# Optimization experiments

Hardware: AMD Instinct MI355X
Metric: run time of the kernel (lower is better)

## Reference

```python
import jax, jax.numpy as jnp
import numpy as np

H = 512   # hidden_dim
K = 6     # n_subclusters
N = 4096  # number of stocks
C = 16    # current_n_clusters


def setup_inputs() -> dict:
    key = jax.random.key(0)
    ks = jax.random.split(key, 12)
    s = 1.0 / np.sqrt(H)
    inp = {
        "stock_embs": jax.random.normal(ks[0], (N, H), jnp.float32),
        "soft_cluster_weights": jax.random.uniform(ks[1], (N, C), jnp.float32),
        "latent_subsegment_assignments": jax.random.uniform(ks[2], (N, C, K), jnp.float32),
        "current_n_clusters": C,
        "Wq": jax.random.normal(ks[3], (H, H), jnp.float32) * s,
        "bq": jnp.zeros((H,), jnp.float32),
        "Wk": jax.random.normal(ks[4], (H, H), jnp.float32) * s,
        "bk": jnp.zeros((H,), jnp.float32),
        "Wv": jax.random.normal(ks[5], (H, H), jnp.float32) * s,
        "bv": jnp.zeros((H,), jnp.float32),
        "Wo": jax.random.normal(ks[6], (H, H), jnp.float32) * s,
        "bo": jnp.zeros((H,), jnp.float32),
        "ln_gamma": jnp.ones((K, H), jnp.float32),
        "ln_beta": jnp.zeros((K, H), jnp.float32),
    }
    return inp


def reference(stock_embs, soft_cluster_weights, latent_subsegment_assignments,
              current_n_clusters, Wq, bq, Wk, bk, Wv, bv, Wo, bo,
              ln_gamma, ln_beta):
    cc = current_n_clusters  # python int, static
    # Mask synthesis: sum_c (w_i w_j)(s_i s_j) == A_k @ A_k^T with A_k = w * s[:,:,k]
    A = soft_cluster_weights[:, :cc, None] * latent_subsegment_assignments[:, :cc, :]  # [N,cc,K]
    masks = jnp.einsum('nck,mck->knm', A, A)                      # [K,N,N]
    masks = masks / (jnp.max(masks, axis=(1, 2), keepdims=True) + 1e-8)
    masks = jnp.log(masks + 1e-10)

    # Projections (dropout is identity in eval mode)
    q = (stock_embs @ Wq.T + bq) / jnp.sqrt(jnp.float32(H))       # [N,H]
    k = stock_embs @ Wk.T + bk                                     # [N,H]
    v = stock_embs @ Wv.T + bv                                     # [N,H]
    scores = q @ k.T                                               # [N,N]

    attn = jax.nn.softmax(scores[None, :, :] + masks, axis=-1)     # [K,N,N]
    ctx = jnp.einsum('knm,md->knd', attn, v)                       # [K,N,H]
    out = ctx @ Wo.T + bo + stock_embs[None, :, :]                 # residual add

    # Per-subcluster LayerNorm (eps=1e-12)
    mu = jnp.mean(out, axis=-1, keepdims=True)
    var = jnp.mean((out - mu) ** 2, axis=-1, keepdims=True)
    out = (out - mu) / jnp.sqrt(var + 1e-12)
    out = out * ln_gamma[:, None, :] + ln_beta[:, None, :]         # [K,N,H]
    return out
```

## Files before the change

### kernel.cpp

```cpp
#include <hip/hip_runtime.h>


typedef _Float16 f16;
typedef _Float16 v8h __attribute__((ext_vector_type(8)));
typedef _Float16 v4h __attribute__((ext_vector_type(4)));
typedef float f32x4 __attribute__((ext_vector_type(4)));

#define MFMA_F16(a, b, c) __builtin_amdgcn_mfma_f32_16x16x32_f16(a, b, c, 0, 0, 0)

#define GLOAD16(gp, lp)                                                        \
  __builtin_amdgcn_global_load_lds(                                            \
      (const __attribute__((address_space(1))) void*)(gp),                     \
      (__attribute__((address_space(3))) void*)(lp), 16, 0, 0)


__global__ void cvt_f16_kernel(const float* __restrict__ in, f16* __restrict__ out, int n4) {
  int i = blockIdx.x * blockDim.x + threadIdx.x;
  if (i < n4) {
    float4 v = ((const float4*)in)[i];
    v4h o = {(f16)v.x, (f16)v.y, (f16)v.z, (f16)v.w};
    ((v4h*)out)[i] = o;
  }
}

__global__ void build_A_kernel(const float* __restrict__ wgt, const float* __restrict__ lat,
                               const int* __restrict__ ccp, f16* __restrict__ Ab, int total) {
  int idx = blockIdx.x * blockDim.x + threadIdx.x;
  if (idx >= total) return;
  int cc = ccp[0];
  int k = idx >> 17;
  int rem = idx & 131071;
  int n = rem >> 5;
  int c = rem & 31;
  float v = 0.f;
  if (c < cc) v = wgt[n * 16 + c] * lat[(n * 16 + c) * 6 + k];
  Ab[idx] = (f16)v;
}

__global__ void diag_max_kernel(const f16* __restrict__ Ab, unsigned* __restrict__ gmax) {
  int idx = blockIdx.x * 256 + threadIdx.x;
  int kk = idx >> 12;
  const v8h* p = (const v8h*)(Ab + (size_t)idx * 32);
  float s = 0.f;
#pragma unroll
  for (int q = 0; q < 4; ++q) {
    v8h a = p[q];
#pragma unroll
    for (int j = 0; j < 8; ++j) s += (float)a[j] * (float)a[j];
  }
#pragma unroll
  for (int msk = 1; msk < 64; msk <<= 1) s = fmaxf(s, __shfl_xor(s, msk, 64));
  if ((threadIdx.x & 63) == 0) atomicMax(&gmax[kk], __float_as_uint(s));
}


template <int MODE>
__global__ __launch_bounds__(256, 2) void gemm_bt(
    const f16* __restrict__ A, const f16* __restrict__ B,
    const float* __restrict__ bias, const float* __restrict__ resid,
    float* __restrict__ outf, f16* __restrict__ outh,
    int M, int Nn, int Kd, int ldo, float alpha) {
  __shared__ f16 As[128 * 32];
  __shared__ f16 Bs[128 * 32];
  const int t = threadIdx.x;
  const int w = t >> 6, lane = t & 63, r15 = lane & 15, r4 = lane >> 4;
  const int wr = w >> 1, wc = w & 1;
  const int row0 = blockIdx.x * 128, col0 = blockIdx.y * 128;

  f32x4 acc[4][4] = {};
  const f16* Ap = A + (size_t)(row0 + (t >> 2)) * Kd + (t & 3) * 8;
  const f16* Bp = B + (size_t)(col0 + (t >> 2)) * Kd + (t & 3) * 8;

  for (int k0 = 0; k0 < Kd; k0 += 32) {
    __syncthreads();
    GLOAD16(Ap + k0, &As[t * 8]);
    GLOAD16(Ap + k0 + (size_t)64 * Kd, &As[2048 + t * 8]);
    GLOAD16(Bp + k0, &Bs[t * 8]);
    GLOAD16(Bp + k0 + (size_t)64 * Kd, &Bs[2048 + t * 8]);
    __syncthreads();
    v8h a[4], b[4];
#pragma unroll
    for (int f = 0; f < 4; ++f) a[f] = *(const v8h*)&As[(wr * 64 + f * 16 + r15) * 32 + r4 * 8];
#pragma unroll
    for (int f = 0; f < 4; ++f) b[f] = *(const v8h*)&Bs[(wc * 64 + f * 16 + r15) * 32 + r4 * 8];
#pragma unroll
    for (int i = 0; i < 4; ++i)
#pragma unroll
      for (int j = 0; j < 4; ++j) acc[i][j] = MFMA_F16(a[i], b[j], acc[i][j]);
  }

#pragma unroll
  for (int i = 0; i < 4; ++i) {
#pragma unroll
    for (int j = 0; j < 4; ++j) {
#pragma unroll
      for (int r = 0; r < 4; ++r) {
        int row = row0 + wr * 64 + i * 16 + r4 * 4 + r;
        int col = col0 + wc * 64 + j * 16 + r15;
        float v = acc[i][j][r];
        if constexpr (MODE == 0) {
          outh[(size_t)row * ldo + col] = (f16)((v + bias[col]) * alpha);
        } else if constexpr (MODE == 1) {
          float vv = v + bias[col];
          size_t idx = (size_t)col * 4096 + (size_t)(row & ~31) + (size_t)((row & 31) ^ ((col & 3) << 3));
          outh[idx] = (f16)vv;
        } else if constexpr (MODE == 3) {
          outf[(size_t)row * ldo + col] = v + bias[col] + resid[(size_t)(row & 4095) * ldo + col];
        } else {
          outh[(size_t)row * ldo + col] = (f16)v;
        }
      }
    }
  }
}

__global__ __launch_bounds__(256) void rowmax_exp_kernel(const f16* __restrict__ scores,
                                                         f16* __restrict__ Eexp) {
  const int row = blockIdx.x, t = threadIdx.x;
  const v8h* src = (const v8h*)(scores + (size_t)row * 4096);
  v8h v0 = src[t], v1 = src[t + 256];
  float m = -3.4e38f;
#pragma unroll
  for (int j = 0; j < 8; ++j) m = fmaxf(m, fmaxf((float)v0[j], (float)v1[j]));
#pragma unroll
  for (int msk = 1; msk < 64; msk <<= 1) m = fmaxf(m, __shfl_xor(m, msk, 64));
  __shared__ float red[4];
  const int w = t >> 6, lane = t & 63;
  if (lane == 0) red[w] = m;
  __syncthreads();
  m = fmaxf(fmaxf(red[0], red[1]), fmaxf(red[2], red[3]));
  v8h o0, o1;
#pragma unroll
  for (int j = 0; j < 8; ++j) {
    o0[j] = (f16)__expf((float)v0[j] - m);
    o1[j] = (f16)__expf((float)v1[j] - m);
  }
  v8h* dst = (v8h*)(Eexp + (size_t)row * 4096);
  dst[t] = o0;
  dst[t + 256] = o1;
}

__global__ __launch_bounds__(512, 2) void attn_pv_kernel(
    const f16* __restrict__ Eexp, const f16* __restrict__ VT,
    const f16* __restrict__ Ab, const unsigned* __restrict__ gmax,
    f16* __restrict__ ctx) {
  __shared__ f16 Vt_s[512 * 32];
  __shared__ f16 E_s[64 * 32];
  __shared__ f16 P_s[64 * 32];
  __shared__ f16 Ar_s[64 * 32];
  __shared__ f16 Ac_s[32 * 32];
  __shared__ float denom_s[128];

  const int t = threadIdx.x;
  const int w = t >> 6, lane = t & 63, r15 = lane & 15, r4 = lane >> 4;
  const int fn = w & 3, fm = w >> 2;

  int d = blockIdx.x + gridDim.x * blockIdx.y;
  int l = (d & 7) * 48 + (d >> 3);
  int r_tile = l / 6;
  int kk = l - r_tile * 6;
  const int row0 = r_tile * 64;

  const float inv = 1.f / (__uint_as_float(gmax[kk]) + 1e-8f);

  f32x4 acc[4][4] = {};
  float dpart[4] = {0.f, 0.f, 0.f, 0.f};
  f32x4 zero4 = {};

  if (t < 256)
    GLOAD16(Ab + ((size_t)(kk * 4096 + row0 + (t >> 2))) * 32 + (t & 3) * 8, &Ar_s[t * 8]);

  for (int mc = 0; mc < 128; ++mc) {
    const int m0 = mc * 32;
#pragma unroll
    for (int i = 0; i < 4; ++i)
      GLOAD16(VT + ((size_t)(i * 128 + (t >> 2))) * 4096 + m0 + (t & 3) * 8, &Vt_s[i * 4096 + t * 8]);
    if (t < 256)
      GLOAD16(Eexp + ((size_t)(row0 + (t >> 2))) * 4096 + m0 + (t & 3) * 8, &E_s[t * 8]);
    if (t < 128)
      GLOAD16(Ab + ((size_t)(kk * 4096 + m0 + (t >> 2))) * 32 + (t & 3) * 8, &Ac_s[t * 8]);
    __syncthreads();
    v8h ga = *(const v8h*)&Ar_s[(fn * 16 + r15) * 32 + r4 * 8];
    v8h gb = *(const v8h*)&Ac_s[(fm * 16 + r15) * 32 + r4 * 8];
    f32x4 g = MFMA_F16(ga, gb, zero4);
#pragma unroll
    for (int r = 0; r < 4; ++r) {
      int nl = fn * 16 + r4 * 4 + r;
      int ml = fm * 16 + r15;
      float e = (float)E_s[nl * 32 + ml];
      float p = e * (g[r] * inv + 1e-10f);
      dpart[r] += p;
      P_s[nl * 32 + (ml ^ ((nl & 3) << 3))] = (f16)p;
    }
    __syncthreads();
    v8h pa[4], vb[4];
#pragma unroll
    for (int f = 0; f < 4; ++f) {
      int n2 = f * 16 + r15;
      pa[f] = *(const v8h*)&P_s[n2 * 32 + ((r4 * 8) ^ ((n2 & 3) << 3))];
      int hl = w * 64 + f * 16 + r15;
      vb[f] = *(const v8h*)&Vt_s[hl * 32 + ((r4 * 8) ^ ((hl & 3) << 3))];
    }
#pragma unroll
    for (int i = 0; i < 4; ++i)
#pragma unroll
      for (int j = 0; j < 4; ++j) acc[i][j] = MFMA_F16(pa[i], vb[j], acc[i][j]);
    __syncthreads();
  }

#pragma unroll
  for (int r = 0; r < 4; ++r) {
#pragma unroll
    for (int msk = 1; msk < 16; msk <<= 1) dpart[r] += __shfl_xor(dpart[r], msk, 64);
  }
  if (r15 == 0) {
#pragma unroll
    for (int r = 0; r < 4; ++r) denom_s[fm * 64 + fn * 16 + r4 * 4 + r] = dpart[r];
  }
  __syncthreads();
#pragma unroll
  for (int i = 0; i < 4; ++i) {
#pragma unroll
    for (int r = 0; r < 4; ++r) {
      int n = i * 16 + r4 * 4 + r;
      float invd = 1.f / (denom_s[n] + denom_s[64 + n]);
#pragma unroll
      for (int j = 0; j < 4; ++j) {
        ctx[((size_t)(kk * 4096 + row0 + n)) * 512 + w * 64 + j * 16 + r15] =
            (f16)(acc[i][j][r] * invd);
      }
    }
  }
}

__global__ __launch_bounds__(256) void ln_kernel(float* __restrict__ out,
                                                 const float* __restrict__ g,
                                                 const float* __restrict__ b) {
  const int row = blockIdx.x, t = threadIdx.x;
  const int k = row >> 12;
  float* base = out + (size_t)row * 512;
  float2 x = ((float2*)base)[t];
  float s = x.x + x.y, sq = x.x * x.x + x.y * x.y;
#pragma unroll
  for (int m = 1; m < 64; m <<= 1) {
    s += __shfl_xor(s, m, 64);
    sq += __shfl_xor(sq, m, 64);
  }
  __shared__ float S[4], Q[4];
  const int w = t >> 6, lane = t & 63;
  if (lane == 0) { S[w] = s; Q[w] = sq; }
  __syncthreads();
  s = S[0] + S[1] + S[2] + S[3];
  sq = Q[0] + Q[1] + Q[2] + Q[3];
  float mu = s * (1.f / 512.f);
  float var = sq * (1.f / 512.f) - mu * mu;
  float invs = rsqrtf(var + 1e-12f);
  int c0 = 2 * t, c1 = 2 * t + 1;
  float2 y;
  y.x = (x.x - mu) * invs * g[k * 512 + c0] + b[k * 512 + c0];
  y.y = (x.y - mu) * invs * g[k * 512 + c1] + b[k * 512 + c1];
  ((float2*)base)[t] = y;
}

extern "C" void kernel_launch(void* const* d_in, const int* in_sizes, int n_in,
                              void* d_out, int out_size, void* d_ws, size_t ws_size,
                              hipStream_t stream) {
  const float* embs = (const float*)d_in[0];
  const float* scw = (const float*)d_in[1];
  const float* lat = (const float*)d_in[2];
  const int* ccp = (const int*)d_in[3];
  const float* Wq = (const float*)d_in[4];
  const float* bq = (const float*)d_in[5];
  const float* Wk = (const float*)d_in[6];
  const float* bk = (const float*)d_in[7];
  const float* Wv = (const float*)d_in[8];
  const float* bv = (const float*)d_in[9];
  const float* Wo = (const float*)d_in[10];
  const float* bo = (const float*)d_in[11];
  const float* lng = (const float*)d_in[12];
  const float* lnb = (const float*)d_in[13];
  float* out = (float*)d_out;

  char* wsp = (char*)d_ws;
  f16* Eh = (f16*)(wsp);
  f16* Wqh = (f16*)(wsp + 0x400000);
  f16* Wkh = (f16*)(wsp + 0x480000);
  f16* Wvh = (f16*)(wsp + 0x500000);
  f16* Woh = (f16*)(wsp + 0x580000);
  f16* qh = (f16*)(wsp + 0x600000);
  f16* kh = (f16*)(wsp + 0xA00000);
  f16* VT = (f16*)(wsp + 0xE00000);
  f16* Ab = (f16*)(wsp + 0x1200000);
  unsigned* gmax = (unsigned*)(wsp + 0x1380000);
  f16* scores_h = (f16*)(wsp + 0x1400000);
  f16* ctxh = (f16*)(wsp + 0x1400000);
  f16* Eexp = (f16*)(wsp + 0x3400000);

  dim3 b256(256);

  cvt_f16_kernel<<<2048, b256, 0, stream>>>(embs, Eh, 524288);
  cvt_f16_kernel<<<256, b256, 0, stream>>>(Wq, Wqh, 65536);
  cvt_f16_kernel<<<256, b256, 0, stream>>>(Wk, Wkh, 65536);
  cvt_f16_kernel<<<256, b256, 0, stream>>>(Wv, Wvh, 65536);
  cvt_f16_kernel<<<256, b256, 0, stream>>>(Wo, Woh, 65536);
  build_A_kernel<<<3072, b256, 0, stream>>>(scw, lat, ccp, Ab, 786432);
  hipMemsetAsync(gmax, 0, 64, stream);

  const float qscale = 0.044194173824159216f;
  gemm_bt<0><<<dim3(32, 4), b256, 0, stream>>>(Eh, Wqh, bq, nullptr, nullptr, qh,
                                               4096, 512, 512, 512, qscale);
  gemm_bt<0><<<dim3(32, 4), b256, 0, stream>>>(Eh, Wkh, bk, nullptr, nullptr, kh,
                                               4096, 512, 512, 512, 1.f);
  gemm_bt<1><<<dim3(32, 4), b256, 0, stream>>>(Eh, Wvh, bv, nullptr, nullptr, VT,
                                               4096, 512, 512, 512, 1.f);
  gemm_bt<4><<<dim3(32, 32), b256, 0, stream>>>(qh, kh, nullptr, nullptr, nullptr, scores_h,
                                                4096, 4096, 512, 4096, 1.f);
  diag_max_kernel<<<96, b256, 0, stream>>>(Ab, gmax);
  rowmax_exp_kernel<<<4096, b256, 0, stream>>>(scores_h, Eexp);
  attn_pv_kernel<<<dim3(64, 6), 512, 0, stream>>>(Eexp, VT, Ab, gmax, ctxh);
  gemm_bt<3><<<dim3(192, 4), b256, 0, stream>>>(ctxh, Woh, bo, embs, out, nullptr,
                                                24576, 512, 512, 512, 1.f);
  ln_kernel<<<24576, b256, 0, stream>>>(out, lng, lnb);
}
```

Before: 420.6 us.

## Fuse conversions, QKV projections, diag-max, and Wo+LayerNorm; double-buffer attention kernel

```diff
diff --git a/kernel.cpp b/kernel.cpp
--- a/kernel.cpp
+++ b/kernel.cpp
@@ -13,20 +13,56 @@
       (const __attribute__((address_space(1))) void*)(gp),                     \
       (__attribute__((address_space(3))) void*)(lp), 16, 0, 0)
 
-
-__global__ void cvt_f16_kernel(const float* __restrict__ in, f16* __restrict__ out, int n4) {
-  int i = blockIdx.x * blockDim.x + threadIdx.x;
-  if (i < n4) {
-    float4 v = ((const float4*)in)[i];
+#define FENCE asm volatile("" ::: "memory")
+#define WAIT_LGKM0                                                             \
+  {                                                                            \
+    asm volatile("s_waitcnt lgkmcnt(0)" ::: "memory");                         \
+    __builtin_amdgcn_sched_barrier(0);                                         \
+  }
+#define WAIT_VM0                                                               \
+  {                                                                            \
+    asm volatile("s_waitcnt vmcnt(0)" ::: "memory");                           \
+    __builtin_amdgcn_sched_barrier(0);                                         \
+  }
+#define BARRIER                                                                \
+  {                                                                            \
+    FENCE;                                                                     \
+    __builtin_amdgcn_s_barrier();                                              \
+    FENCE;                                                                     \
+    __builtin_amdgcn_sched_barrier(0);                                         \
+  }
+
+__global__ void cvt_all_kernel(const float* __restrict__ embs,
+                               const float* __restrict__ Wq, const float* __restrict__ Wk,
+                               const float* __restrict__ Wv, const float* __restrict__ Wo,
+                               const float* __restrict__ bq, const float* __restrict__ bk,
+                               const float* __restrict__ bv,
+                               f16* __restrict__ Eh, f16* __restrict__ Wcat,
+                               float* __restrict__ bcat) {
+  int i = blockIdx.x * 256 + threadIdx.x;
+  if (i < 524288) {
+    float4 v = ((const float4*)embs)[i];
     v4h o = {(f16)v.x, (f16)v.y, (f16)v.z, (f16)v.w};
-    ((v4h*)out)[i] = o;
+    ((v4h*)Eh)[i] = o;
+  } else if (i < 786432) {
+    int widx = i - 524288;
+    int r = widx >> 16;
+    const float* src = (r == 0) ? Wq : (r == 1) ? Wk : (r == 2) ? Wv : Wo;
+    float4 v = ((const float4*)src)[widx & 65535];
+    v4h o = {(f16)v.x, (f16)v.y, (f16)v.z, (f16)v.w};
+    ((v4h*)Wcat)[widx] = o;
+  } else if (i < 786816) {
+    int bidx = i - 786432;
+    int r = bidx >> 7;
+    const float* src = (r == 0) ? bq : (r == 1) ? bk : bv;
+    ((float4*)bcat)[bidx] = ((const float4*)src)[bidx & 127];
   }
 }
 
 __global__ void build_A_kernel(const float* __restrict__ wgt, const float* __restrict__ lat,
-                               const int* __restrict__ ccp, f16* __restrict__ Ab, int total) {
-  int idx = blockIdx.x * blockDim.x + threadIdx.x;
-  if (idx >= total) return;
+                               const int* __restrict__ ccp, f16* __restrict__ Ab,
+                               unsigned* __restrict__ gmax) {
+  int idx = blockIdx.x * 256 + threadIdx.x;
   int cc = ccp[0];
   int k = idx >> 17;
   int rem = idx & 131071;
@@ -34,32 +70,28 @@
   int c = rem & 31;
   float v = 0.f;
   if (c < cc) v = wgt[n * 16 + c] * lat[(n * 16 + c) * 6 + k];
-  Ab[idx] = (f16)v;
-}
-
-__global__ void diag_max_kernel(const f16* __restrict__ Ab, unsigned* __restrict__ gmax) {
-  int idx = blockIdx.x * 256 + threadIdx.x;
-  int kk = idx >> 12;
-  const v8h* p = (const v8h*)(Ab + (size_t)idx * 32);
-  float s = 0.f;
-#pragma unroll
-  for (int q = 0; q < 4; ++q) {
-    v8h a = p[q];
-#pragma unroll
-    for (int j = 0; j < 8; ++j) s += (float)a[j] * (float)a[j];
-  }
-#pragma unroll
-  for (int msk = 1; msk < 64; msk <<= 1) s = fmaxf(s, __shfl_xor(s, msk, 64));
-  if ((threadIdx.x & 63) == 0) atomicMax(&gmax[kk], __float_as_uint(s));
-}
-
+  f16 h = (f16)v;
+  Ab[idx] = h;
+  float fv = (float)h;
+  float s = fv * fv;
+#pragma unroll
+  for (int m = 1; m <= 16; m <<= 1) s += __shfl_xor(s, m, 64);
+  s = fmaxf(s, __shfl_xor(s, 32, 64));
+  __shared__ float red[4];
+  int t = threadIdx.x, w = t >> 6;
+  if ((t & 63) == 0) red[w] = s;
+  __syncthreads();
+  if (t == 0) {
+    float m4 = fmaxf(fmaxf(red[0], red[1]), fmaxf(red[2], red[3]));
+    atomicMax(&gmax[k], __float_as_uint(m4));
+  }
+}
 
 template <int MODE>
 __global__ __launch_bounds__(256, 2) void gemm_bt(
     const f16* __restrict__ A, const f16* __restrict__ B,
-    const float* __restrict__ bias, const float* __restrict__ resid,
-    float* __restrict__ outf, f16* __restrict__ outh,
-    int M, int Nn, int Kd, int ldo, float alpha) {
+    const float* __restrict__ bias, f16* __restrict__ outh, f16* __restrict__ aux,
+    int Kd, int ldo, float alpha) {
   __shared__ f16 As[128 * 32];
   __shared__ f16 Bs[128 * 32];
   const int t = threadIdx.x;
@@ -98,16 +130,19 @@
         int row = row0 + wr * 64 + i * 16 + r4 * 4 + r;
         int col = col0 + wc * 64 + j * 16 + r15;
         float v = acc[i][j][r];
-        if constexpr (MODE == 0) {
-          outh[(size_t)row * ldo + col] = (f16)((v + bias[col]) * alpha);
-        } else if constexpr (MODE == 1) {
+        if constexpr (MODE == 4) {
+          outh[(size_t)row * ldo + col] = (f16)v;
+        } else {
           float vv = v + bias[col];
-          size_t idx = (size_t)col * 4096 + (size_t)(row & ~31) + (size_t)((row & 31) ^ ((col & 3) << 3));
-          outh[idx] = (f16)vv;
-        } else if constexpr (MODE == 3) {
-          outf[(size_t)row * ldo + col] = v + bias[col] + resid[(size_t)(row & 4095) * ldo + col];
-        } else {
-          outh[(size_t)row * ldo + col] = (f16)v;
+          int reg = col >> 9;
+          if (reg < 2) {
+            float sc = (reg == 0) ? alpha : 1.f;
+            outh[(size_t)reg * 2097152 + (size_t)row * 512 + (col & 511)] = (f16)(vv * sc);
+          } else {
+            int cv = col & 511;
+            aux[(size_t)cv * 4096 + (size_t)(row & ~31) + (size_t)((row & 31) ^ ((cv & 3) << 3))] =
+                (f16)vv;
+          }
         }
       }
     }
@@ -140,72 +175,99 @@
   dst[t + 256] = o1;
 }
 
-__global__ __launch_bounds__(512, 2) void attn_pv_kernel(
+__global__ __launch_bounds__(256, 3) void attn_pv2_kernel(
     const f16* __restrict__ Eexp, const f16* __restrict__ VT,
     const f16* __restrict__ Ab, const unsigned* __restrict__ gmax,
     f16* __restrict__ ctx) {
-  __shared__ f16 Vt_s[512 * 32];
-  __shared__ f16 E_s[64 * 32];
+  __shared__ f16 Vt_s[2][256 * 32];
+  __shared__ f16 E_s[2][64 * 32];
   __shared__ f16 P_s[64 * 32];
-  __shared__ f16 Ar_s[64 * 32];
-  __shared__ f16 Ac_s[32 * 32];
-  __shared__ float denom_s[128];
+  __shared__ float denom_s[64];
 
   const int t = threadIdx.x;
   const int w = t >> 6, lane = t & 63, r15 = lane & 15, r4 = lane >> 4;
-  const int fn = w & 3, fm = w >> 2;
-
-  int d = blockIdx.x + gridDim.x * blockIdx.y;
-  int l = (d & 7) * 48 + (d >> 3);
-  int r_tile = l / 6;
-  int kk = l - r_tile * 6;
-  const int row0 = r_tile * 64;
+
+  int d = blockIdx.x;
+  int xcd = d & 7, jj6 = d >> 3;
+  int strip = xcd * 8 + jj6 / 12;
+  int sub = jj6 % 12;
+  int hh = sub / 6, kk = sub - (sub / 6) * 6;
+  const int row0 = strip * 64;
+  const int h0 = hh * 256;
 
   const float inv = 1.f / (__uint_as_float(gmax[kk]) + 1e-8f);
+  const f16* Abk = Ab + (size_t)kk * 4096 * 32;
+
+  v8h ga = *(const v8h*)(Abk + (size_t)(row0 + w * 16 + r15) * 32 + r4 * 8);
 
   f32x4 acc[4][4] = {};
   float dpart[4] = {0.f, 0.f, 0.f, 0.f};
   f32x4 zero4 = {};
 
-  if (t < 256)
-    GLOAD16(Ab + ((size_t)(kk * 4096 + row0 + (t >> 2))) * 32 + (t & 3) * 8, &Ar_s[t * 8]);
-
-  for (int mc = 0; mc < 128; ++mc) {
-    const int m0 = mc * 32;
-#pragma unroll
-    for (int i = 0; i < 4; ++i)
-      GLOAD16(VT + ((size_t)(i * 128 + (t >> 2))) * 4096 + m0 + (t & 3) * 8, &Vt_s[i * 4096 + t * 8]);
-    if (t < 256)
-      GLOAD16(Eexp + ((size_t)(row0 + (t >> 2))) * 4096 + m0 + (t & 3) * 8, &E_s[t * 8]);
-    if (t < 128)
-      GLOAD16(Ab + ((size_t)(kk * 4096 + m0 + (t >> 2))) * 32 + (t & 3) * 8, &Ac_s[t * 8]);
-    __syncthreads();
-    v8h ga = *(const v8h*)&Ar_s[(fn * 16 + r15) * 32 + r4 * 8];
-    v8h gb = *(const v8h*)&Ac_s[(fm * 16 + r15) * 32 + r4 * 8];
-    f32x4 g = MFMA_F16(ga, gb, zero4);
-#pragma unroll
-    for (int r = 0; r < 4; ++r) {
-      int nl = fn * 16 + r4 * 4 + r;
-      int ml = fm * 16 + r15;
-      float e = (float)E_s[nl * 32 + ml];
-      float p = e * (g[r] * inv + 1e-10f);
-      dpart[r] += p;
-      P_s[nl * 32 + (ml ^ ((nl & 3) << 3))] = (f16)p;
-    }
-    __syncthreads();
-    v8h pa[4], vb[4];
-#pragma unroll
-    for (int f = 0; f < 4; ++f) {
-      int n2 = f * 16 + r15;
-      pa[f] = *(const v8h*)&P_s[n2 * 32 + ((r4 * 8) ^ ((n2 & 3) << 3))];
-      int hl = w * 64 + f * 16 + r15;
-      vb[f] = *(const v8h*)&Vt_s[hl * 32 + ((r4 * 8) ^ ((hl & 3) << 3))];
-    }
-#pragma unroll
-    for (int i = 0; i < 4; ++i)
-#pragma unroll
-      for (int j = 0; j < 4; ++j) acc[i][j] = MFMA_F16(pa[i], vb[j], acc[i][j]);
-    __syncthreads();
+#define ATTN_STAGE(P, M0S)                                                     \
+  {                                                                            \
+    _Pragma("unroll") for (int i2 = 0; i2 < 4; ++i2)                           \
+        GLOAD16(VT + (size_t)(h0 + i2 * 64 + (t >> 2)) * 4096 + (M0S) + (t & 3) * 8, \
+                &Vt_s[P][i2 * 2048 + t * 8]);                                  \
+    {                                                                          \
+      int nn = t >> 2;                                                         \
+      int cs = (t & 3) ^ ((nn >> 2) & 3);                                      \
+      GLOAD16(Eexp + (size_t)(row0 + nn) * 4096 + (M0S) + cs * 8, &E_s[P][t * 8]); \
+    }                                                                          \
+  }
+
+#define ATTN_COMPUTE(P, GB)                                                    \
+  {                                                                            \
+    f32x4 g0 = MFMA_F16(ga, GB[0], zero4);                                     \
+    f32x4 g1 = MFMA_F16(ga, GB[1], zero4);                                     \
+    _Pragma("unroll") for (int r = 0; r < 4; ++r) {                            \
+      int nl = w * 16 + r4 * 4 + r;                                            \
+      int xo = r4 << 3;                                                        \
+      float e0 = (float)E_s[P][nl * 32 + (r15 ^ xo)];                          \
+      float e1 = (float)E_s[P][nl * 32 + ((16 + r15) ^ xo)];                   \
+      float p0 = e0 * (g0[r] * inv + 1e-10f);                                  \
+      float p1 = e1 * (g1[r] * inv + 1e-10f);                                  \
+      dpart[r] += p0 + p1;                                                     \
+      P_s[nl * 32 + (r15 ^ xo)] = (f16)p0;                                     \
+      P_s[nl * 32 + ((16 + r15) ^ xo)] = (f16)p1;                              \
+    }                                                                          \
+    WAIT_LGKM0;                                                                \
+    BARRIER;                                                                   \
+    v8h pa[4], vb[4];                                                          \
+    _Pragma("unroll") for (int f = 0; f < 4; ++f) {                            \
+      int n2 = f * 16 + r15;                                                   \
+      pa[f] = *(const v8h*)&P_s[n2 * 32 + ((r4 * 8) ^ (((n2 >> 2) & 3) << 3))];\
+      int hl = w * 64 + f * 16 + r15;                                          \
+      vb[f] = *(const v8h*)&Vt_s[P][hl * 32 + ((r4 * 8) ^ ((hl & 3) << 3))];   \
+    }                                                                          \
+    __builtin_amdgcn_s_setprio(1);                                             \
+    _Pragma("unroll") for (int i = 0; i < 4; ++i)                              \
+        _Pragma("unroll") for (int j2 = 0; j2 < 4; ++j2)                       \
+            acc[i][j2] = MFMA_F16(pa[i], vb[j2], acc[i][j2]);                  \
+    __builtin_amdgcn_s_setprio(0);                                             \
+    WAIT_LGKM0;                                                                \
+    WAIT_VM0;                                                                  \
+    BARRIER;                                                                   \
+  }
+
+  ATTN_STAGE(0, 0);
+  v8h gb0[2], gb1[2];
+  gb0[0] = *(const v8h*)(Abk + (size_t)(0 + r15) * 32 + r4 * 8);
+  gb0[1] = *(const v8h*)(Abk + (size_t)(16 + r15) * 32 + r4 * 8);
+  WAIT_VM0;
+  BARRIER;
+
+  for (int mc = 0; mc < 128; mc += 2) {
+    int mn = (mc + 1) * 32;
+    ATTN_STAGE(1, mn);
+    gb1[0] = *(const v8h*)(Abk + (size_t)(mn + r15) * 32 + r4 * 8);
+    gb1[1] = *(const v8h*)(Abk + (size_t)(mn + 16 + r15) * 32 + r4 * 8);
+    ATTN_COMPUTE(0, gb0);
+    int mn2 = (mc + 2 < 128) ? (mc + 2) * 32 : 0;
+    ATTN_STAGE(0, mn2);
+    gb0[0] = *(const v8h*)(Abk + (size_t)(mn2 + r15) * 32 + r4 * 8);
+    gb0[1] = *(const v8h*)(Abk + (size_t)(mn2 + 16 + r15) * 32 + r4 * 8);
+    ATTN_COMPUTE(1, gb1);
   }
 
 #pragma unroll
@@ -215,7 +277,7 @@
   }
   if (r15 == 0) {
 #pragma unroll
-    for (int r = 0; r < 4; ++r) denom_s[fm * 64 + fn * 16 + r4 * 4 + r] = dpart[r];
+    for (int r = 0; r < 4; ++r) denom_s[w * 16 + r4 * 4 + r] = dpart[r];
   }
   __syncthreads();
 #pragma unroll
@@ -223,43 +285,144 @@
 #pragma unroll
     for (int r = 0; r < 4; ++r) {
       int n = i * 16 + r4 * 4 + r;
-      float invd = 1.f / (denom_s[n] + denom_s[64 + n]);
+      float invd = 1.f / denom_s[n];
 #pragma unroll
       for (int j = 0; j < 4; ++j) {
-        ctx[((size_t)(kk * 4096 + row0 + n)) * 512 + w * 64 + j * 16 + r15] =
+        ctx[((size_t)(kk * 4096 + row0 + n)) * 512 + h0 + w * 64 + j * 16 + r15] =
             (f16)(acc[i][j][r] * invd);
       }
     }
   }
-}
-
-__global__ __launch_bounds__(256) void ln_kernel(float* __restrict__ out,
-                                                 const float* __restrict__ g,
-                                                 const float* __restrict__ b) {
-  const int row = blockIdx.x, t = threadIdx.x;
-  const int k = row >> 12;
-  float* base = out + (size_t)row * 512;
-  float2 x = ((float2*)base)[t];
-  float s = x.x + x.y, sq = x.x * x.x + x.y * x.y;
-#pragma unroll
-  for (int m = 1; m < 64; m <<= 1) {
-    s += __shfl_xor(s, m, 64);
-    sq += __shfl_xor(sq, m, 64);
-  }
-  __shared__ float S[4], Q[4];
-  const int w = t >> 6, lane = t & 63;
-  if (lane == 0) { S[w] = s; Q[w] = sq; }
+#undef ATTN_STAGE
+#undef ATTN_COMPUTE
+}
+
+__global__ __launch_bounds__(512, 4) void wo_ln_kernel(
+    const f16* __restrict__ ctxh, const f16* __restrict__ Woh,
+    const float* __restrict__ bo, const float* __restrict__ embs,
+    const float* __restrict__ lng, const float* __restrict__ lnb,
+    float* __restrict__ out) {
+  __shared__ f16 As_[2][48 * 32];
+  __shared__ f16 Bs_[2][512 * 32];
+  __shared__ float redS[8][48];
+  __shared__ float redQ[8][48];
+  __shared__ float muS[48], ivS[48];
+
+  const int t = threadIdx.x;
+  const int w = t >> 6, lane = t & 63, r15 = lane & 15, r4 = lane >> 4;
+  const int row0 = blockIdx.x * 48;
+  const int wm3 = w % 3;
+  const int caRow = wm3 * 64 + lane;
+
+  f32x4 acc[3][4] = {};
+
+#define WO_STAGE(P, KQ)                                                        \
+  {                                                                            \
+    GLOAD16(ctxh + (size_t)(row0 + (caRow >> 2)) * 512 + (KQ) + (caRow & 3) * 8, \
+            &As_[P][caRow * 8]);                                               \
+    _Pragma("unroll") for (int q2 = 0; q2 < 4; ++q2)                           \
+        GLOAD16(Woh + (size_t)((q2 * 512 + t) >> 2) * 512 + (KQ) + (t & 3) * 8,\
+                &Bs_[P][(q2 * 512 + t) * 8]);                                  \
+  }
+
+#define WO_COMPUTE(P)                                                          \
+  {                                                                            \
+    v8h a[3], b[4];                                                            \
+    _Pragma("unroll") for (int i = 0; i < 3; ++i)                              \
+        a[i] = *(const v8h*)&As_[P][(i * 16 + r15) * 32 + r4 * 8];             \
+    _Pragma("unroll") for (int j = 0; j < 4; ++j)                              \
+        b[j] = *(const v8h*)&Bs_[P][(w * 64 + j * 16 + r15) * 32 + r4 * 8];    \
+    __builtin_amdgcn_s_setprio(1);                                             \
+    _Pragma("unroll") for (int i = 0; i < 3; ++i)                              \
+        _Pragma("unroll") for (int j = 0; j < 4; ++j)                          \
+            acc[i][j] = MFMA_F16(a[i], b[j], acc[i][j]);                       \
+    __builtin_amdgcn_s_setprio(0);                                             \
+    WAIT_LGKM0;                                                                \
+    WAIT_VM0;                                                                  \
+    BARRIER;                                                                   \
+  }
+
+  WO_STAGE(0, 0);
+  WAIT_VM0;
+  BARRIER;
+  for (int kq = 0; kq < 16; kq += 2) {
+    WO_STAGE(1, (kq + 1) * 32);
+    WO_COMPUTE(0);
+    int k2 = (kq + 2 < 16) ? (kq + 2) * 32 : 0;
+    WO_STAGE(0, k2);
+    WO_COMPUTE(1);
+  }
+#undef WO_STAGE
+#undef WO_COMPUTE
+
+  float sS[3][4], sQ[3][4];
+#pragma unroll
+  for (int i = 0; i < 3; ++i) {
+#pragma unroll
+    for (int r = 0; r < 4; ++r) {
+      int R = row0 + i * 16 + r4 * 4 + r;
+      int er = R & 4095;
+      float s = 0.f, q = 0.f;
+#pragma unroll
+      for (int j = 0; j < 4; ++j) {
+        int col = w * 64 + j * 16 + r15;
+        float v = acc[i][j][r] + bo[col] + embs[(size_t)er * 512 + col];
+        acc[i][j][r] = v;
+        s += v;
+        q += v * v;
+      }
+      sS[i][r] = s;
+      sQ[i][r] = q;
+    }
+  }
+#pragma unroll
+  for (int i = 0; i < 3; ++i)
+#pragma unroll
+    for (int r = 0; r < 4; ++r)
+#pragma unroll
+      for (int msk = 1; msk < 16; msk <<= 1) {
+        sS[i][r] += __shfl_xor(sS[i][r], msk, 64);
+        sQ[i][r] += __shfl_xor(sQ[i][r], msk, 64);
+      }
+  if (r15 == 0) {
+#pragma unroll
+    for (int i = 0; i < 3; ++i)
+#pragma unroll
+      for (int r = 0; r < 4; ++r) {
+        redS[w][i * 16 + r4 * 4 + r] = sS[i][r];
+        redQ[w][i * 16 + r4 * 4 + r] = sQ[i][r];
+      }
+  }
   __syncthreads();
-  s = S[0] + S[1] + S[2] + S[3];
-  sq = Q[0] + Q[1] + Q[2] + Q[3];
-  float mu = s * (1.f / 512.f);
-  float var = sq * (1.f / 512.f) - mu * mu;
-  float invs = rsqrtf(var + 1e-12f);
-  int c0 = 2 * t, c1 = 2 * t + 1;
-  float2 y;
-  y.x = (x.x - mu) * invs * g[k * 512 + c0] + b[k * 512 + c0];
-  y.y = (x.y - mu) * invs * g[k * 512 + c1] + b[k * 512 + c1];
-  ((float2*)base)[t] = y;
+  if (t < 48) {
+    float s = 0.f, q = 0.f;
+#pragma unroll
+    for (int wv = 0; wv < 8; ++wv) {
+      s += redS[wv][t];
+      q += redQ[wv][t];
+    }
+    float mu = s * (1.f / 512.f);
+    float var = q * (1.f / 512.f) - mu * mu;
+    muS[t] = mu;
+    ivS[t] = rsqrtf(var + 1e-12f);
+  }
+  __syncthreads();
+#pragma unroll
+  for (int i = 0; i < 3; ++i) {
+#pragma unroll
+    for (int r = 0; r < 4; ++r) {
+      int n = i * 16 + r4 * 4 + r;
+      int R = row0 + n;
+      int k = R >> 12;
+      float mu = muS[n], iv = ivS[n];
+#pragma unroll
+      for (int j = 0; j < 4; ++j) {
+        int col = w * 64 + j * 16 + r15;
+        out[(size_t)R * 512 + col] =
+            (acc[i][j][r] - mu) * iv * lng[k * 512 + col] + lnb[k * 512 + col];
+      }
+    }
+  }
 }
 
 extern "C" void kernel_launch(void* const* d_in, const int* in_sizes, int n_in,
@@ -283,42 +446,29 @@
 
   char* wsp = (char*)d_ws;
   f16* Eh = (f16*)(wsp);
-  f16* Wqh = (f16*)(wsp + 0x400000);
-  f16* Wkh = (f16*)(wsp + 0x480000);
-  f16* Wvh = (f16*)(wsp + 0x500000);
+  f16* Wcat = (f16*)(wsp + 0x400000);
   f16* Woh = (f16*)(wsp + 0x580000);
   f16* qh = (f16*)(wsp + 0x600000);
-  f16* kh = (f16*)(wsp + 0xA00000);
   f16* VT = (f16*)(wsp + 0xE00000);
   f16* Ab = (f16*)(wsp + 0x1200000);
   unsigned* gmax = (unsigned*)(wsp + 0x1380000);
+  float* bcat = (float*)(wsp + 0x1381000);
   f16* scores_h = (f16*)(wsp + 0x1400000);
   f16* ctxh = (f16*)(wsp + 0x1400000);
   f16* Eexp = (f16*)(wsp + 0x3400000);
 
   dim3 b256(256);
-
-  cvt_f16_kernel<<<2048, b256, 0, stream>>>(embs, Eh, 524288);
-  cvt_f16_kernel<<<256, b256, 0, stream>>>(Wq, Wqh, 65536);
-  cvt_f16_kernel<<<256, b256, 0, stream>>>(Wk, Wkh, 65536);
-  cvt_f16_kernel<<<256, b256, 0, stream>>>(Wv, Wvh, 65536);
-  cvt_f16_kernel<<<256, b256, 0, stream>>>(Wo, Woh, 65536);
-  build_A_kernel<<<3072, b256, 0, stream>>>(scw, lat, ccp, Ab, 786432);
+  const float qscale = 0.044194173824159216f;
+
   hipMemsetAsync(gmax, 0, 64, stream);
-
-  const float qscale = 0.044194173824159216f;
-  gemm_bt<0><<<dim3(32, 4), b256, 0, stream>>>(Eh, Wqh, bq, nullptr, nullptr, qh,
-                                               4096, 512, 512, 512, qscale);
-  gemm_bt<0><<<dim3(32, 4), b256, 0, stream>>>(Eh, Wkh, bk, nullptr, nullptr, kh,
-                                               4096, 512, 512, 512, 1.f);
-  gemm_bt<1><<<dim3(32, 4), b256, 0, stream>>>(Eh, Wvh, bv, nullptr, nullptr, VT,
-                                               4096, 512, 512, 512, 1.f);
-  gemm_bt<4><<<dim3(32, 32), b256, 0, stream>>>(qh, kh, nullptr, nullptr, nullptr, scores_h,
-                                                4096, 4096, 512, 4096, 1.f);
-  diag_max_kernel<<<96, b256, 0, stream>>>(Ab, gmax);
+  cvt_all_kernel<<<3074, b256, 0, stream>>>(embs, Wq, Wk, Wv, Wo, bq, bk, bv,
+                                            Eh, Wcat, bcat);
+  build_A_kernel<<<3072, b256, 0, stream>>>(scw, lat, ccp, Ab, gmax);
+  gemm_bt<5><<<dim3(32, 12), b256, 0, stream>>>(Eh, Wcat, bcat, qh, VT,
+                                                512, 512, qscale);
+  gemm_bt<4><<<dim3(32, 32), b256, 0, stream>>>(qh, qh + 2097152, nullptr, scores_h,
+                                                nullptr, 512, 4096, 1.f);
   rowmax_exp_kernel<<<4096, b256, 0, stream>>>(scores_h, Eexp);
-  attn_pv_kernel<<<dim3(64, 6), 512, 0, stream>>>(Eexp, VT, Ab, gmax, ctxh);
-  gemm_bt<3><<<dim3(192, 4), b256, 0, stream>>>(ctxh, Woh, bo, embs, out, nullptr,
-                                                24576, 512, 512, 512, 1.f);
-  ln_kernel<<<24576, b256, 0, stream>>>(out, lng, lnb);
-}
+  attn_pv2_kernel<<<768, b256, 0, stream>>>(Eexp, VT, Ab, gmax, ctxh);
+  wo_ln_kernel<<<512, 512, 0, stream>>>(ctxh, Woh, bo, embs, lng, lnb, out);
+}
```

New measurement: 413.8 us. Within noise of the previous version (-1.6%).
